# Kernel tuning notes

Measured on AMD Instinct MI355X. Metric: run time of the kernel, lower is better.

## Reference

```python
import jax, jax.numpy as jnp
import numpy as np

SM_SCALE = 0.07216878364870322  # 1/sqrt(192)
PAGE_SIZE = 64


def setup_inputs() -> dict:
    key = jax.random.key(0)
    ks = jax.random.split(key, 6)
    B, Hq, Hkv = 32, 16, 1
    DN, DR, DV = 128, 64, 128
    NUM_PAGES, MAX_PAGES = 2048, 64
    return {
        "q": jax.random.normal(ks[0], (B, Hq, DN + DR), dtype=jnp.float32),
        "k_nope_buffer": jax.random.normal(ks[1], (NUM_PAGES, PAGE_SIZE, Hkv, DN), dtype=jnp.float32),
        "k_rope_buffer": jax.random.normal(ks[2], (NUM_PAGES, PAGE_SIZE, Hkv, DR), dtype=jnp.float32),
        "v_buffer": jax.random.normal(ks[3], (NUM_PAGES, PAGE_SIZE, Hkv, DV), dtype=jnp.float32),
        "seq_lens": jax.random.randint(ks[4], (B,), 1, MAX_PAGES * PAGE_SIZE + 1, dtype=jnp.int32),
        "block_table": jax.random.randint(ks[5], (B, MAX_PAGES), 0, NUM_PAGES, dtype=jnp.int32),
    }


def reference(q, k_nope_buffer, k_rope_buffer, v_buffer, seq_lens, block_table):
    B, Hq, _ = q.shape
    Hkv = k_nope_buffer.shape[2]
    dn = k_nope_buffer.shape[-1]
    dv = v_buffer.shape[-1]
    max_kv = block_table.shape[1] * PAGE_SIZE

    q_nope = q[:, :, :dn]            # (B, Hq, dn)
    q_rope = q[:, :, dn:]            # (B, Hq, dr)

    # Gather pages per batch: (B, max_pages, page, Hkv, d) -> (B, max_kv, Hkv, d)
    kn = k_nope_buffer[block_table].reshape(B, max_kv, Hkv, dn)
    kr = k_rope_buffer[block_table].reshape(B, max_kv, Hkv, -1)
    v = v_buffer[block_table].reshape(B, max_kv, Hkv, dv)

    rep = Hq // Hkv  # GQA repeat_interleave == repeat along head axis
    if rep != 1:
        kn = jnp.repeat(kn, rep, axis=2)
        kr = jnp.repeat(kr, rep, axis=2)
        v = jnp.repeat(v, rep, axis=2)

    scores = (jnp.einsum('bhd,bkhd->bhk', q_nope, kn)
              + jnp.einsum('bhd,bkhd->bhk', q_rope, kr)).astype(jnp.float32) * SM_SCALE
    # Mask out key positions beyond each sequence length (replaces per-batch slicing)
    valid = jnp.arange(max_kv)[None, None, :] < seq_lens[:, None, None]
    scores = jnp.where(valid, scores, -jnp.inf)
    probs = jax.nn.softmax(scores, axis=-1).astype(v.dtype)  # (B, Hq, max_kv)
    out = jnp.einsum('bhk,bkhd->bhd', probs, v)              # (B, Hq, dv)
    return out
```

## Files before the change

### kernel.cpp

```cpp
#include <hip/hip_runtime.h>
#include <math.h>

#define NB 32
#define HQ 16
#define DN 128
#define DR 64
#define DQ (DN + DR)
#define DV 128
#define PAGE 64
#define MAXP 64
#define SM_SCALE 0.07216878364870322f
#define RS 88

typedef __attribute__((ext_vector_type(8))) _Float16 f16x8;
typedef __attribute__((ext_vector_type(4))) _Float16 f16x4;
typedef __attribute__((ext_vector_type(2))) __fp16   h16x2;
typedef __attribute__((ext_vector_type(4))) float    f32x4;

union F16x8 { f16x8 v; h16x2 h[4]; };
union F16x4 { f16x4 v; h16x2 h[2]; };

template<int NSC>
__global__ __launch_bounds__(256, 2)
void attn_partial_kernel(const float* __restrict__ q,
                         const float* __restrict__ kn,
                         const float* __restrict__ kr,
                         const float* __restrict__ v,
                         const int* __restrict__ seq_lens,
                         const int* __restrict__ block_table,
                         float* __restrict__ o_part,
                         float* __restrict__ ml_part)
{
    const int tid  = (int)threadIdx.x;
    const int wave = tid >> 6;
    const int lane = tid & 63;
    const int ln   = lane & 15;
    const int qd   = lane >> 4;

    const int item = blockIdx.x * 4 + wave;
    const int b = item / NSC;
    const int c = item % NSC;

    const int seq = seq_lens[b];
    if (c * PAGE >= seq) return;

    __shared__ _Float16 p_s[4][HQ][RS];

    F16x8 bq[6];
    {
        const float* qrow = q + ((size_t)b * HQ + ln) * DQ + qd * 8;
        #pragma unroll
        for (int kt = 0; kt < 6; kt++) {
            float4 x0 = *(const float4*)(qrow + kt * 32);
            float4 x1 = *(const float4*)(qrow + kt * 32 + 4);
            bq[kt].h[0] = __builtin_amdgcn_cvt_pkrtz(x0.x, x0.y);
            bq[kt].h[1] = __builtin_amdgcn_cvt_pkrtz(x0.z, x0.w);
            bq[kt].h[2] = __builtin_amdgcn_cvt_pkrtz(x1.x, x1.y);
            bq[kt].h[3] = __builtin_amdgcn_cvt_pkrtz(x1.z, x1.w);
        }
    }

    float m_run = -INFINITY, l_run = 0.f;
    f32x4 o_acc[8];
    #pragma unroll
    for (int i = 0; i < 8; i++) o_acc[i] = (f32x4){0.f, 0.f, 0.f, 0.f};

    #pragma unroll
    for (int pg = 0; pg < MAXP / NSC; pg++) {
        const int page = c + pg * NSC;
        if (page * PAGE >= seq) break;
        const int pid = block_table[b * MAXP + page];

        f32x4 sc[4];
        #pragma unroll
        for (int mt = 0; mt < 4; mt++) sc[mt] = (f32x4){0.f, 0.f, 0.f, 0.f};
        const float* knb = kn + (size_t)pid * PAGE * DN;
        const float* krb = kr + (size_t)pid * PAGE * DR;
        #pragma unroll
        for (int mt = 0; mt < 4; mt++) {
            const float* rn = knb + (mt * 16 + ln) * DN + qd * 8;
            const float* rr = krb + (mt * 16 + ln) * DR + qd * 8;
            #pragma unroll
            for (int kt = 0; kt < 6; kt++) {
                const float* src = (kt < 4) ? (rn + kt * 32) : (rr + (kt - 4) * 32);
                float4 x0 = *(const float4*)(src);
                float4 x1 = *(const float4*)(src + 4);
                F16x8 a;
                a.h[0] = __builtin_amdgcn_cvt_pkrtz(x0.x, x0.y);
                a.h[1] = __builtin_amdgcn_cvt_pkrtz(x0.z, x0.w);
                a.h[2] = __builtin_amdgcn_cvt_pkrtz(x1.x, x1.y);
                a.h[3] = __builtin_amdgcn_cvt_pkrtz(x1.z, x1.w);
                sc[mt] = __builtin_amdgcn_mfma_f32_16x16x32_f16(a.v, bq[kt].v, sc[mt], 0, 0, 0);
            }
        }

        float sv[4][4];
        float smax = -INFINITY;
        #pragma unroll
        for (int mt = 0; mt < 4; mt++)
            #pragma unroll
            for (int r = 0; r < 4; r++) {
                int tok = page * PAGE + mt * 16 + qd * 4 + r;
                float x = (tok < seq) ? sc[mt][r] * SM_SCALE : -INFINITY;
                sv[mt][r] = x;
                smax = fmaxf(smax, x);
            }
        smax = fmaxf(smax, __shfl_xor(smax, 16));
        smax = fmaxf(smax, __shfl_xor(smax, 32));
        const float m_new = fmaxf(m_run, smax);
        const float alpha = __expf(m_run - m_new);
        m_run = m_new;
        float lsum = 0.f;
        #pragma unroll
        for (int mt = 0; mt < 4; mt++)
            #pragma unroll
            for (int r = 0; r < 4; r++) {
                float e = __expf(sv[mt][r] - m_new);
                sv[mt][r] = e;
                lsum += e;
            }
        lsum += __shfl_xor(lsum, 16);
        lsum += __shfl_xor(lsum, 32);
        l_run = l_run * alpha + lsum;

        #pragma unroll
        for (int mt = 0; mt < 4; mt++) {
            F16x4 w;
            w.h[0] = __builtin_amdgcn_cvt_pkrtz(sv[mt][0], sv[mt][1]);
            w.h[1] = __builtin_amdgcn_cvt_pkrtz(sv[mt][2], sv[mt][3]);
            *(f16x4*)(&p_s[wave][ln][mt * 16 + qd * 4]) = w.v;
        }

        #pragma unroll
        for (int i = 0; i < 8; i++) o_acc[i] *= alpha;

        const float* vb = v + (size_t)pid * PAGE * DV;
        #pragma unroll
        for (int kt2 = 0; kt2 < 2; kt2++) {
            f16x8 pf = *(const f16x8*)(&p_s[wave][ln][kt2 * 32 + qd * 8]);
            const int t0 = kt2 * 32 + qd * 8;
            #pragma unroll
            for (int mt2 = 0; mt2 < 8; mt2++) {
                const float* vc = vb + mt2 * 16 + ln;
                F16x8 a;
                a.h[0] = __builtin_amdgcn_cvt_pkrtz(vc[(t0 + 0) * DV], vc[(t0 + 1) * DV]);
                a.h[1] = __builtin_amdgcn_cvt_pkrtz(vc[(t0 + 2) * DV], vc[(t0 + 3) * DV]);
                a.h[2] = __builtin_amdgcn_cvt_pkrtz(vc[(t0 + 4) * DV], vc[(t0 + 5) * DV]);
                a.h[3] = __builtin_amdgcn_cvt_pkrtz(vc[(t0 + 6) * DV], vc[(t0 + 7) * DV]);
                o_acc[mt2] = __builtin_amdgcn_mfma_f32_16x16x32_f16(a.v, pf, o_acc[mt2], 0, 0, 0);
            }
        }
    }

    float* op = o_part + ((size_t)(b * NSC + c) * HQ + ln) * DV + qd * 4;
    #pragma unroll
    for (int mt2 = 0; mt2 < 8; mt2++)
        *(f32x4*)(op + mt2 * 16) = o_acc[mt2];
    if (qd == 0) {
        float2* ml = (float2*)(ml_part) + (size_t)(b * NSC + c) * HQ + ln;
        *ml = make_float2(m_run, l_run);
    }
}

template<int NSC>
__global__ __launch_bounds__(128)
void attn_combine_kernel(const float* __restrict__ o_part,
                         const float* __restrict__ ml_part,
                         const int* __restrict__ seq_lens,
                         float* __restrict__ out)
{
    const int h = blockIdx.x;
    const int b = blockIdx.y;
    const int d = (int)threadIdx.x;
    const int seq = seq_lens[b];
    int npages = (seq + PAGE - 1) / PAGE;
    int ns = npages < NSC ? npages : NSC;

    const float2* mlb = (const float2*)(ml_part) + (size_t)b * NSC * HQ + h;
    float M = -INFINITY;
    #pragma unroll 8
    for (int s2 = 0; s2 < ns; s2++)
        M = fmaxf(M, mlb[(size_t)s2 * HQ].x);

    float acc = 0.f, den = 0.f;
    #pragma unroll 4
    for (int s2 = 0; s2 < ns; s2++) {
        float2 ml = mlb[(size_t)s2 * HQ];
        float e = __expf(ml.x - M);
        float o = o_part[((size_t)(b * NSC + s2) * HQ + h) * DV + d];
        acc += e * o;
        den += e * ml.y;
    }
    out[((size_t)b * HQ + h) * DV + d] = acc / den;
}

extern "C" void kernel_launch(void* const* d_in, const int* in_sizes, int n_in,
                              void* d_out, int out_size, void* d_ws, size_t ws_size,
                              hipStream_t stream)
{
    const float* q  = (const float*)d_in[0];
    const float* kn = (const float*)d_in[1];
    const float* kr = (const float*)d_in[2];
    const float* v  = (const float*)d_in[3];
    const int* seq_lens    = (const int*)d_in[4];
    const int* block_table = (const int*)d_in[5];

    const size_t need32 = (size_t)NB * 32 * HQ * (DV + 2) * 4;
    if (ws_size >= need32) {
        constexpr int NSC = 32;
        float* o_part  = (float*)d_ws;
        float* ml_part = o_part + (size_t)NB * NSC * HQ * DV;
        attn_partial_kernel<NSC><<<NB * NSC / 4, 256, 0, stream>>>(
            q, kn, kr, v, seq_lens, block_table, o_part, ml_part);
        attn_combine_kernel<NSC><<<dim3(HQ, NB), 128, 0, stream>>>(
            o_part, ml_part, seq_lens, (float*)d_out);
    } else {
        constexpr int NSC = 16;
        float* o_part  = (float*)d_ws;
        float* ml_part = o_part + (size_t)NB * NSC * HQ * DV;
        attn_partial_kernel<NSC><<<NB * NSC / 4, 256, 0, stream>>>(
            q, kn, kr, v, seq_lens, block_table, o_part, ml_part);
        attn_combine_kernel<NSC><<<dim3(HQ, NB), 128, 0, stream>>>(
            o_part, ml_part, seq_lens, (float*)d_out);
    }
}
```

Baseline: 216.9 us.

## Use one-wave blocks, prefetch V into registers, and split up to 64 ways

Each partial-attention block now holds a single 64-lane wave instead of four, so the LDS buffer for P shrinks to one tile. The V loads for a page are issued into registers before the softmax so their latency overlaps with the score reduction. A new 64-way split-KV path is used when the workspace is large enough, which spreads each sequence over more blocks. The trade-off is much higher register pressure from the 128-float V prefetch, plus more partial results for the combine kernel to merge.

```diff
diff --git a/kernel.cpp b/kernel.cpp
--- a/kernel.cpp
+++ b/kernel.cpp
@@ -20,8 +20,10 @@
 union F16x8 { f16x8 v; h16x2 h[4]; };
 union F16x4 { f16x4 v; h16x2 h[2]; };
 
+#define WAVE_LDS_FENCE() asm volatile("s_waitcnt lgkmcnt(0)" ::: "memory")
+
 template<int NSC>
-__global__ __launch_bounds__(256, 2)
+__global__ __launch_bounds__(64, 1)
 void attn_partial_kernel(const float* __restrict__ q,
                          const float* __restrict__ kn,
                          const float* __restrict__ kr,
@@ -31,20 +33,17 @@
                          float* __restrict__ o_part,
                          float* __restrict__ ml_part)
 {
-    const int tid  = (int)threadIdx.x;
-    const int wave = tid >> 6;
-    const int lane = tid & 63;
+    const int lane = (int)threadIdx.x;
     const int ln   = lane & 15;
     const int qd   = lane >> 4;
 
-    const int item = blockIdx.x * 4 + wave;
-    const int b = item / NSC;
-    const int c = item % NSC;
+    const int b = blockIdx.x / NSC;
+    const int c = blockIdx.x % NSC;
 
     const int seq = seq_lens[b];
     if (c * PAGE >= seq) return;
 
-    __shared__ _Float16 p_s[4][HQ][RS];
+    __shared__ _Float16 p_s[HQ][RS];
 
     F16x8 bq[6];
     {
@@ -71,11 +70,13 @@
         if (page * PAGE >= seq) break;
         const int pid = block_table[b * MAXP + page];
 
-        f32x4 sc[4];
-        #pragma unroll
-        for (int mt = 0; mt < 4; mt++) sc[mt] = (f32x4){0.f, 0.f, 0.f, 0.f};
         const float* knb = kn + (size_t)pid * PAGE * DN;
         const float* krb = kr + (size_t)pid * PAGE * DR;
+        const float* vb  = v  + (size_t)pid * PAGE * DV;
+
+        f32x4 sc[4];
+        #pragma unroll
+        for (int mt = 0; mt < 4; mt++) sc[mt] = (f32x4){0.f, 0.f, 0.f, 0.f};
         #pragma unroll
         for (int mt = 0; mt < 4; mt++) {
             const float* rn = knb + (mt * 16 + ln) * DN + qd * 8;
@@ -94,6 +95,19 @@
             }
         }
 
+        float vraw[16][8];
+        #pragma unroll
+        for (int kt2 = 0; kt2 < 2; kt2++) {
+            const int t0 = kt2 * 32 + qd * 8;
+            #pragma unroll
+            for (int mt2 = 0; mt2 < 8; mt2++) {
+                const float* vc = vb + mt2 * 16 + ln;
+                #pragma unroll
+                for (int j = 0; j < 8; j++)
+                    vraw[kt2 * 8 + mt2][j] = vc[(size_t)(t0 + j) * DV];
+            }
+        }
+
         float sv[4][4];
         float smax = -INFINITY;
         #pragma unroll
@@ -123,30 +137,30 @@
         lsum += __shfl_xor(lsum, 32);
         l_run = l_run * alpha + lsum;
 
+        WAVE_LDS_FENCE();
         #pragma unroll
         for (int mt = 0; mt < 4; mt++) {
             F16x4 w;
             w.h[0] = __builtin_amdgcn_cvt_pkrtz(sv[mt][0], sv[mt][1]);
             w.h[1] = __builtin_amdgcn_cvt_pkrtz(sv[mt][2], sv[mt][3]);
-            *(f16x4*)(&p_s[wave][ln][mt * 16 + qd * 4]) = w.v;
-        }
+            *(f16x4*)(&p_s[ln][mt * 16 + qd * 4]) = w.v;
+        }
+        WAVE_LDS_FENCE();
 
         #pragma unroll
         for (int i = 0; i < 8; i++) o_acc[i] *= alpha;
 
-        const float* vb = v + (size_t)pid * PAGE * DV;
         #pragma unroll
         for (int kt2 = 0; kt2 < 2; kt2++) {
-            f16x8 pf = *(const f16x8*)(&p_s[wave][ln][kt2 * 32 + qd * 8]);
-            const int t0 = kt2 * 32 + qd * 8;
+            f16x8 pf = *(const f16x8*)(&p_s[ln][kt2 * 32 + qd * 8]);
             #pragma unroll
             for (int mt2 = 0; mt2 < 8; mt2++) {
-                const float* vc = vb + mt2 * 16 + ln;
+                const float* vr = vraw[kt2 * 8 + mt2];
                 F16x8 a;
-                a.h[0] = __builtin_amdgcn_cvt_pkrtz(vc[(t0 + 0) * DV], vc[(t0 + 1) * DV]);
-                a.h[1] = __builtin_amdgcn_cvt_pkrtz(vc[(t0 + 2) * DV], vc[(t0 + 3) * DV]);
-                a.h[2] = __builtin_amdgcn_cvt_pkrtz(vc[(t0 + 4) * DV], vc[(t0 + 5) * DV]);
-                a.h[3] = __builtin_amdgcn_cvt_pkrtz(vc[(t0 + 6) * DV], vc[(t0 + 7) * DV]);
+                a.h[0] = __builtin_amdgcn_cvt_pkrtz(vr[0], vr[1]);
+                a.h[1] = __builtin_amdgcn_cvt_pkrtz(vr[2], vr[3]);
+                a.h[2] = __builtin_amdgcn_cvt_pkrtz(vr[4], vr[5]);
+                a.h[3] = __builtin_amdgcn_cvt_pkrtz(vr[6], vr[7]);
                 o_acc[mt2] = __builtin_amdgcn_mfma_f32_16x16x32_f16(a.v, pf, o_acc[mt2], 0, 0, 0);
             }
         }
@@ -194,6 +208,19 @@
     out[((size_t)b * HQ + h) * DV + d] = acc / den;
 }
 
+template<int NSC>
+static void launch_all(const float* q, const float* kn, const float* kr,
+                       const float* v, const int* seq_lens, const int* block_table,
+                       float* d_ws, float* d_out, hipStream_t stream)
+{
+    float* o_part  = d_ws;
+    float* ml_part = o_part + (size_t)NB * NSC * HQ * DV;
+    attn_partial_kernel<NSC><<<NB * NSC, 64, 0, stream>>>(
+        q, kn, kr, v, seq_lens, block_table, o_part, ml_part);
+    attn_combine_kernel<NSC><<<dim3(HQ, NB), 128, 0, stream>>>(
+        o_part, ml_part, seq_lens, d_out);
+}
+
 extern "C" void kernel_launch(void* const* d_in, const int* in_sizes, int n_in,
                               void* d_out, int out_size, void* d_ws, size_t ws_size,
                               hipStream_t stream)
@@ -205,22 +232,13 @@
     const int* seq_lens    = (const int*)d_in[4];
     const int* block_table = (const int*)d_in[5];
 
+    const size_t need64 = (size_t)NB * 64 * HQ * (DV + 2) * 4;
     const size_t need32 = (size_t)NB * 32 * HQ * (DV + 2) * 4;
-    if (ws_size >= need32) {
-        constexpr int NSC = 32;
-        float* o_part  = (float*)d_ws;
-        float* ml_part = o_part + (size_t)NB * NSC * HQ * DV;
-        attn_partial_kernel<NSC><<<NB * NSC / 4, 256, 0, stream>>>(
-            q, kn, kr, v, seq_lens, block_table, o_part, ml_part);
-        attn_combine_kernel<NSC><<<dim3(HQ, NB), 128, 0, stream>>>(
-            o_part, ml_part, seq_lens, (float*)d_out);
-    } else {
-        constexpr int NSC = 16;
-        float* o_part  = (float*)d_ws;
-        float* ml_part = o_part + (size_t)NB * NSC * HQ * DV;
-        attn_partial_kernel<NSC><<<NB * NSC / 4, 256, 0, stream>>>(
-            q, kn, kr, v, seq_lens, block_table, o_part, ml_part);
-        attn_combine_kernel<NSC><<<dim3(HQ, NB), 128, 0, stream>>>(
-            o_part, ml_part, seq_lens, (float*)d_out);
-    }
-}
+
+    if (ws_size >= need64)
+        launch_all<64>(q, kn, kr, v, seq_lens, block_table, (float*)d_ws, (float*)d_out, stream);
+    else if (ws_size >= need32)
+        launch_all<32>(q, kn, kr, v, seq_lens, block_table, (float*)d_ws, (float*)d_out, stream);
+    else
+        launch_all<16>(q, kn, kr, v, seq_lens, block_table, (float*)d_ws, (float*)d_out, stream);
+}
```

New measurement: 185.1 us. 14.6% less time.
